# Performance work log

Hardware: AMD Instinct MI355X
Metric: run time of the kernel (lower is better)

Reference implementation:

```python
import jax, jax.numpy as jnp
import numpy as np

C = 512
C8 = C // 8   # query/key dim = 64
C2 = C // 2   # value dim = 256


def setup_inputs() -> dict:
    key = jax.random.key(0)
    ks = jax.random.split(key, 10)
    B, H, W = 4, 64, 64
    x = jax.random.normal(ks[0], (B, H, W, C), dtype=jnp.float32)
    # 1x1 conv kernels expressed as [in_ch, out_ch] matrices + biases
    Wf = jax.random.normal(ks[1], (C, C8), dtype=jnp.float32) * 0.02
    bf = jnp.zeros((C8,), dtype=jnp.float32)
    Wg = jax.random.normal(ks[2], (C, C8), dtype=jnp.float32) * 0.02
    bg = jnp.zeros((C8,), dtype=jnp.float32)
    Wh = jax.random.normal(ks[3], (C, C2), dtype=jnp.float32) * 0.02
    bh = jnp.zeros((C2,), dtype=jnp.float32)
    Wo = jax.random.normal(ks[4], (C2, C), dtype=jnp.float32) * 0.02
    bo = jnp.zeros((C,), dtype=jnp.float32)
    gamma = jax.random.normal(ks[5], (1,), dtype=jnp.float32) * 0.05
    return {"x": x, "Wf": Wf, "bf": bf, "Wg": Wg, "bg": bg,
            "Wh": Wh, "bh": bh, "Wo": Wo, "bo": bo, "gamma": gamma}


def reference(x, Wf, bf, Wg, bg, Wh, bh, Wo, bo, gamma):
    B, H, W, _ = x.shape
    N = H * W
    xf = x.reshape(B, N, C)                               # flatten spatial dims
    f = xf @ Wf + bf                                      # [B, N, C8] keys
    g = xf @ Wg + bg                                      # [B, N, C8] queries
    h = xf @ Wh + bh                                      # [B, N, C2] values
    s = jnp.einsum('bnd,bmd->bnm', g, f)                  # [B, N, N] scores (g @ f^T)
    beta = jax.nn.softmax(s, axis=-1)                     # attention map
    o = jnp.einsum('bnm,bmd->bnd', beta, h)               # [B, N, C2]
    o = o @ Wo + bo                                       # [B, N, C] output 1x1 conv
    out = gamma * o + xf                                  # residual with learned scale
    return out.reshape(B, H, W, C)
```

## Files before the change

kernel.cpp:

```cpp
#include <hip/hip_runtime.h>
#include <math.h>

#define B_   4
#define N_   4096
#define C_   512
#define C8_  64
#define C2_  256

typedef __attribute__((ext_vector_type(8))) short bf16x8;
typedef __attribute__((ext_vector_type(4))) short bf16x4;
typedef __attribute__((ext_vector_type(4))) float floatx4;
typedef __attribute__((ext_vector_type(16))) float floatx16;

__device__ __forceinline__ short f2bf(float x) {
    unsigned u = __float_as_uint(x);
    u += 0x7fff + ((u >> 16) & 1);
    return (short)(u >> 16);
}
__device__ __forceinline__ unsigned pack2bf(float a, float b) {
    return (unsigned)(unsigned short)f2bf(a) | ((unsigned)(unsigned short)f2bf(b) << 16);
}

union U8 { bf16x8 v; unsigned u[4]; };

__global__ __launch_bounds__(256) void convert_w(
    const float* __restrict__ Wf, const float* __restrict__ Wg,
    const float* __restrict__ Wh, const float* __restrict__ Wo,
    short* __restrict__ WcatT, short* __restrict__ WoT)
{
    int tid = blockIdx.x * 256 + threadIdx.x;
    if (tid < 384 * 512) {
        int n = tid >> 9, k = tid & 511;
        float v = (n < 64)  ? Wf[k * 64 + n]
                : (n < 128) ? Wg[k * 64 + (n - 64)]
                            : Wh[k * 256 + (n - 128)];
        WcatT[tid] = f2bf(v);
    } else {
        int t2 = tid - 384 * 512;
        int n = t2 >> 8, k = t2 & 255;
        WoT[t2] = f2bf(Wo[k * 512 + n]);
    }
}

__global__ __launch_bounds__(256, 2) void qkv_mfma(
    const float* __restrict__ x, const short* __restrict__ WcatT,
    const float* __restrict__ bfv, const float* __restrict__ bgv,
    const float* __restrict__ bhv,
    short* __restrict__ fbf, short* __restrict__ gbf, short* __restrict__ hT)
{
    const int ny = blockIdx.x;
    const int m0 = blockIdx.y * 128;
    const int n0 = ny * 128;
    const int t  = threadIdx.x;
    const int w  = t >> 6, lane = t & 63;
    const int l15 = lane & 15, quad = lane >> 4;
    const int wm = w & 1, wn = w >> 1;

    __shared__ short As[128 * 40];
    __shared__ short Bs[128 * 40];

    floatx4 acc[4][4];
    #pragma unroll
    for (int i = 0; i < 4; i++)
        #pragma unroll
        for (int j = 0; j < 4; j++) acc[i][j] = (floatx4){0.f,0.f,0.f,0.f};

    for (int k0 = 0; k0 < C_; k0 += 32) {
        #pragma unroll
        for (int i = 0; i < 4; i++) {
            int c = t + i * 256;
            int row = c >> 3, ko = (c & 7) * 4;
            float4 v = *(const float4*)&x[(size_t)(m0 + row) * C_ + k0 + ko];
            bf16x4 pk = { f2bf(v.x), f2bf(v.y), f2bf(v.z), f2bf(v.w) };
            *(bf16x4*)&As[row * 40 + ko] = pk;
        }
        #pragma unroll
        for (int i = 0; i < 2; i++) {
            int c = t + i * 256;
            int nr = c >> 2, ko = (c & 3) * 8;
            *(bf16x8*)&Bs[nr * 40 + ko] =
                *(const bf16x8*)&WcatT[(size_t)(n0 + nr) * 512 + k0 + ko];
        }
        __syncthreads();

        bf16x8 af[4], bfr[4];
        #pragma unroll
        for (int mt = 0; mt < 4; mt++)
            af[mt] = *(const bf16x8*)&As[(wm * 64 + mt * 16 + l15) * 40 + quad * 8];
        #pragma unroll
        for (int nt = 0; nt < 4; nt++)
            bfr[nt] = *(const bf16x8*)&Bs[(wn * 64 + nt * 16 + l15) * 40 + quad * 8];
        #pragma unroll
        for (int mt = 0; mt < 4; mt++)
            #pragma unroll
            for (int nt = 0; nt < 4; nt++)
                acc[mt][nt] = __builtin_amdgcn_mfma_f32_16x16x32_bf16(af[mt], bfr[nt], acc[mt][nt], 0, 0, 0);
        __syncthreads();
    }

    if (ny == 0) {
        #pragma unroll
        for (int mt = 0; mt < 4; mt++) {
            #pragma unroll
            for (int nt = 0; nt < 4; nt++) {
                int cn = wn * 64 + nt * 16 + l15;
                #pragma unroll
                for (int rg = 0; rg < 4; rg++) {
                    int row = m0 + wm * 64 + mt * 16 + quad * 4 + rg;
                    float v = acc[mt][nt][rg];
                    if (cn < 64) fbf[(size_t)row * 64 + cn]        = f2bf(v + bfv[cn]);
                    else         gbf[(size_t)row * 64 + (cn - 64)] = f2bf(v + bgv[cn - 64]);
                }
            }
        }
    } else {
        #pragma unroll
        for (int mt = 0; mt < 4; mt++) {
            #pragma unroll
            for (int nt = 0; nt < 4; nt++) {
                int hch = (ny - 1) * 128 + wn * 64 + nt * 16 + l15;
                int row = m0 + wm * 64 + mt * 16 + quad * 4;
                int bb = row >> 12, n = row & 4095;
                float bias = bhv[hch];
                bf16x4 pk = { f2bf(acc[mt][nt][0] + bias), f2bf(acc[mt][nt][1] + bias),
                              f2bf(acc[mt][nt][2] + bias), f2bf(acc[mt][nt][3] + bias) };
                *(bf16x4*)&hT[((size_t)(bb * 256 + hch)) * 4096 + n] = pk;
            }
        }
    }
}

#define HST 40

__global__ __launch_bounds__(256, 1) void attn_v3(
    const short* __restrict__ fK,
    const short* __restrict__ gQ,
    const short* __restrict__ hT,
    float* __restrict__ oPart,
    float* __restrict__ lPart)
{
    const int bx = blockIdx.x;
    const int s  = bx & 1;
    const int qt = (bx >> 1) & 31;
    const int b  = bx >> 6;
    const int kb = s * 2048;
    const int t  = threadIdx.x;
    const int w  = t >> 6, lane = t & 63;
    const int l31 = lane & 31, h = lane >> 5;
    const int wq = w & 1, wv = w >> 1;
    const int q_wave = qt * 128 + wq * 64;

    __shared__ short fs[2][64 * HST];
    __shared__ short hs[2][256 * HST];

    bf16x8 qf[2][4];
    #pragma unroll
    for (int n2 = 0; n2 < 2; n2++)
        #pragma unroll
        for (int k = 0; k < 4; k++)
            qf[n2][k] = *(const bf16x8*)&gQ[(size_t)(b * N_ + q_wave + n2 * 32 + l31) * 64 + k * 16 + h * 8];

    floatx16 oacc[2][4];
    #pragma unroll
    for (int n2 = 0; n2 < 2; n2++)
        #pragma unroll
        for (int vt = 0; vt < 4; vt++)
            #pragma unroll
            for (int j = 0; j < 16; j++) oacc[n2][vt][j] = 0.f;
    float lsum[2] = {0.f, 0.f};

    const int f_row = t >> 2, f_c = (t & 3) * 16;
    const int h_row = t >> 3, h_c = (t & 7) * 8;

    {
        *(bf16x8*)&fs[0][f_row * HST + f_c] =
            *(const bf16x8*)&fK[(size_t)(b * N_ + kb + f_row) * 64 + f_c];
        *(bf16x8*)&fs[0][f_row * HST + f_c + 8] =
            *(const bf16x8*)&fK[(size_t)(b * N_ + kb + f_row) * 64 + f_c + 8];
        #pragma unroll
        for (int i = 0; i < 8; i++)
            *(bf16x8*)&hs[0][(h_row + i * 32) * HST + h_c] =
                *(const bf16x8*)&hT[((size_t)(b * 256 + h_row + i * 32)) * 4096 + kb + h_c];
    }
    __syncthreads();

    for (int it = 0; it < 32; ++it) {
        const int cur = it & 1;
        const bool more = (it < 31);
        const int kn = kb + (it + 1) * 64;

        bf16x8 rf0, rf1, rh[8];
        if (more) {
            rf0 = *(const bf16x8*)&fK[(size_t)(b * N_ + kn + f_row) * 64 + f_c];
            rf1 = *(const bf16x8*)&fK[(size_t)(b * N_ + kn + f_row) * 64 + f_c + 8];
            #pragma unroll
            for (int i = 0; i < 8; i++)
                rh[i] = *(const bf16x8*)&hT[((size_t)(b * 256 + h_row + i * 32)) * 4096 + kn + h_c];
        }

        bf16x8 ffr[2][4];
        #pragma unroll
        for (int m = 0; m < 2; m++)
            #pragma unroll
            for (int k = 0; k < 4; k++)
                ffr[m][k] = *(const bf16x8*)&fs[cur][(m * 32 + l31) * HST + k * 16 + h * 8];

        floatx16 sacc[2][2];
        #pragma unroll
        for (int m = 0; m < 2; m++)
            #pragma unroll
            for (int n2 = 0; n2 < 2; n2++) {
                #pragma unroll
                for (int j = 0; j < 16; j++) sacc[m][n2][j] = 0.f;
                #pragma unroll
                for (int k = 0; k < 4; k++)
                    sacc[m][n2] = __builtin_amdgcn_mfma_f32_32x32x16_bf16(
                        ffr[m][k], qf[n2][k], sacc[m][n2], 0, 0, 0);
            }

        bf16x8 pfrag[2][4];
        #pragma unroll
        for (int m = 0; m < 2; m++)
            #pragma unroll
            for (int n2 = 0; n2 < 2; n2++) {
                float p[16]; float ps_ = 0.f;
                #pragma unroll
                for (int j = 0; j < 16; j++) { p[j] = __expf(sacc[m][n2][j]); ps_ += p[j]; }
                ps_ += __shfl_xor(ps_, 32);
                lsum[n2] += ps_;
                unsigned pk[8], xk[8];
                #pragma unroll
                for (int i = 0; i < 8; i++) pk[i] = pack2bf(p[2 * i], p[2 * i + 1]);
                #pragma unroll
                for (int i = 0; i < 8; i++) xk[i] = __shfl_xor(pk[i], 32);
                #pragma unroll
                for (int kp = 0; kp < 2; kp++) {
                    U8 u;
                    u.u[0] = h ? xk[4 * kp + 2] : pk[4 * kp];
                    u.u[1] = h ? xk[4 * kp + 3] : pk[4 * kp + 1];
                    u.u[2] = h ? pk[4 * kp + 2] : xk[4 * kp];
                    u.u[3] = h ? pk[4 * kp + 3] : xk[4 * kp + 1];
                    pfrag[n2][m * 2 + kp] = u.v;
                }
            }

        #pragma unroll
        for (int kk = 0; kk < 4; kk++)
            #pragma unroll
            for (int vt = 0; vt < 4; vt++) {
                bf16x8 vfr = *(const bf16x8*)&hs[cur][(wv * 128 + vt * 32 + l31) * HST + kk * 16 + h * 8];
                #pragma unroll
                for (int n2 = 0; n2 < 2; n2++)
                    oacc[n2][vt] = __builtin_amdgcn_mfma_f32_32x32x16_bf16(
                        pfrag[n2][kk], vfr, oacc[n2][vt], 0, 0, 0);
            }

        if (more) {
            const int nxt = cur ^ 1;
            *(bf16x8*)&fs[nxt][f_row * HST + f_c] = rf0;
            *(bf16x8*)&fs[nxt][f_row * HST + f_c + 8] = rf1;
            #pragma unroll
            for (int i = 0; i < 8; i++)
                *(bf16x8*)&hs[nxt][(h_row + i * 32) * HST + h_c] = rh[i];
        }
        __syncthreads();
    }

    #pragma unroll
    for (int n2 = 0; n2 < 2; n2++) {
        #pragma unroll
        for (int vt = 0; vt < 4; vt++) {
            int vch = wv * 128 + vt * 32 + l31;
            #pragma unroll
            for (int r = 0; r < 16; r++) {
                int q = q_wave + n2 * 32 + (r & 3) + 8 * (r >> 2) + 4 * h;
                oPart[(size_t)s * 4194304 + (size_t)(b * N_ + q) * 256 + vch] = oacc[n2][vt][r];
            }
        }
    }
    if (wv == 0 && lane < 32) {
        #pragma unroll
        for (int n2 = 0; n2 < 2; n2++)
            lPart[(size_t)s * 16384 + b * N_ + q_wave + n2 * 32 + lane] = lsum[n2];
    }
}

__global__ __launch_bounds__(256) void attn_combine(
    const float* __restrict__ oPart, const float* __restrict__ lPart,
    short* __restrict__ obf)
{
    int idx = blockIdx.x * 256 + threadIdx.x;
    int row = idx >> 6;
    int c4  = (idx & 63) << 2;
    float4 a = *(const float4*)&oPart[(size_t)row * 256 + c4];
    float4 b = *(const float4*)&oPart[4194304 + (size_t)row * 256 + c4];
    float inv = 1.0f / (lPart[row] + lPart[16384 + row]);
    bf16x4 o = { f2bf((a.x + b.x) * inv), f2bf((a.y + b.y) * inv),
                 f2bf((a.z + b.z) * inv), f2bf((a.w + b.w) * inv) };
    *(bf16x4*)&obf[(size_t)row * 256 + c4] = o;
}

__global__ __launch_bounds__(256, 2) void out_mfma(
    const short* __restrict__ obf, const short* __restrict__ WoT,
    const float* __restrict__ bo, const float* __restrict__ x,
    const float* __restrict__ gamma, float* __restrict__ out)
{
    const int n0 = blockIdx.x * 128;
    const int m0 = blockIdx.y * 128;
    const int t  = threadIdx.x;
    const int w  = t >> 6, lane = t & 63;
    const int l15 = lane & 15, quad = lane >> 4;
    const int wm = w & 1, wn = w >> 1;

    __shared__ short As[128 * 40];
    __shared__ short Bs[128 * 40];

    floatx4 acc[4][4];
    #pragma unroll
    for (int i = 0; i < 4; i++)
        #pragma unroll
        for (int j = 0; j < 4; j++) acc[i][j] = (floatx4){0.f,0.f,0.f,0.f};

    for (int k0 = 0; k0 < C2_; k0 += 32) {
        #pragma unroll
        for (int i = 0; i < 2; i++) {
            int c = t + i * 256;
            int row = c >> 2, ko = (c & 3) * 8;
            *(bf16x8*)&As[row * 40 + ko] =
                *(const bf16x8*)&obf[(size_t)(m0 + row) * 256 + k0 + ko];
        }
        #pragma unroll
        for (int i = 0; i < 2; i++) {
            int c = t + i * 256;
            int nr = c >> 2, ko = (c & 3) * 8;
            *(bf16x8*)&Bs[nr * 40 + ko] =
                *(const bf16x8*)&WoT[(size_t)(n0 + nr) * 256 + k0 + ko];
        }
        __syncthreads();

        bf16x8 af[4], bfr[4];
        #pragma unroll
        for (int mt = 0; mt < 4; mt++)
            af[mt] = *(const bf16x8*)&As[(wm * 64 + mt * 16 + l15) * 40 + quad * 8];
        #pragma unroll
        for (int nt = 0; nt < 4; nt++)
            bfr[nt] = *(const bf16x8*)&Bs[(wn * 64 + nt * 16 + l15) * 40 + quad * 8];
        #pragma unroll
        for (int mt = 0; mt < 4; mt++)
            #pragma unroll
            for (int nt = 0; nt < 4; nt++)
                acc[mt][nt] = __builtin_amdgcn_mfma_f32_16x16x32_bf16(af[mt], bfr[nt], acc[mt][nt], 0, 0, 0);
        __syncthreads();
    }

    const float gm = gamma[0];
    #pragma unroll
    for (int mt = 0; mt < 4; mt++) {
        #pragma unroll
        for (int nt = 0; nt < 4; nt++) {
            int col = n0 + wn * 64 + nt * 16 + l15;
            float bias = bo[col];
            #pragma unroll
            for (int rg = 0; rg < 4; rg++) {
                int row = m0 + wm * 64 + mt * 16 + quad * 4 + rg;
                out[(size_t)row * C_ + col] =
                    gm * (acc[mt][nt][rg] + bias) + x[(size_t)row * C_ + col];
            }
        }
    }
}

extern "C" void kernel_launch(void* const* d_in, const int* in_sizes, int n_in,
                              void* d_out, int out_size, void* d_ws, size_t ws_size,
                              hipStream_t stream) {
    (void)in_sizes; (void)n_in; (void)out_size; (void)ws_size;

    const float* x     = (const float*)d_in[0];
    const float* Wf    = (const float*)d_in[1];
    const float* bfv   = (const float*)d_in[2];
    const float* Wg    = (const float*)d_in[3];
    const float* bgv   = (const float*)d_in[4];
    const float* Wh    = (const float*)d_in[5];
    const float* bhv   = (const float*)d_in[6];
    const float* Wo    = (const float*)d_in[7];
    const float* bo    = (const float*)d_in[8];
    const float* gamma = (const float*)d_in[9];
    float* out = (float*)d_out;

    short* fbf   = (short*)d_ws;
    short* gbf   = fbf   + (size_t)B_ * N_ * C8_;
    short* hT    = gbf   + (size_t)B_ * N_ * C8_;
    short* obf   = hT    + (size_t)B_ * C2_ * N_;
    short* WcatT = obf   + (size_t)B_ * N_ * C2_;
    short* WoT   = WcatT + (size_t)384 * 512;
    float* oPart = (float*)(WoT + (size_t)512 * 256);
    float* lPart = oPart + (size_t)2 * 16384 * 256;

    convert_w<<<1280, 256, 0, stream>>>(Wf, Wg, Wh, Wo, WcatT, WoT);
    qkv_mfma<<<dim3(3, 128), 256, 0, stream>>>(x, WcatT, bfv, bgv, bhv, fbf, gbf, hT);
    attn_v3<<<256, 256, 0, stream>>>(fbf, gbf, hT, oPart, lPart);
    attn_combine<<<4096, 256, 0, stream>>>(oPart, lPart, obf);
    out_mfma<<<dim3(4, 128), 256, 0, stream>>>(obf, WoT, bo, x, gamma, out);
}
```

Measured before the change: 231.9 us.

## Split attention keys four ways, store bf16 partials, use exp2 with prescaled queries

The attention kernel now splits the key range into four chunks instead of two, giving 512 blocks, and allows two blocks per CU. Partial outputs are stored as bf16 instead of fp32, and the combine kernel sums four partials. Queries are prescaled by log2(e) so exp2f can replace __expf. P is packed to bf16 with a cheaper round-half-up permute, and the S/PV loop is interleaved per key half to lower register pressure and overlap the LDS stores. The aim is better occupancy and less partial-output traffic, at the cost of extra combine reads and some bf16 rounding in the partials. The softmax still has no max subtraction, as before.

Result: slower. 260.8 us (+12.5%).

```diff
diff --git a/kernel.cpp b/kernel.cpp
--- a/kernel.cpp
+++ b/kernel.cpp
@@ -6,6 +6,7 @@
 #define C_   512
 #define C8_  64
 #define C2_  256
+#define LOG2E 1.44269504f
 
 typedef __attribute__((ext_vector_type(8))) short bf16x8;
 typedef __attribute__((ext_vector_type(4))) short bf16x4;
@@ -17,8 +18,13 @@
     u += 0x7fff + ((u >> 16) & 1);
     return (short)(u >> 16);
 }
-__device__ __forceinline__ unsigned pack2bf(float a, float b) {
-    return (unsigned)(unsigned short)f2bf(a) | ((unsigned)(unsigned short)f2bf(b) << 16);
+__device__ __forceinline__ unsigned pack2bf_fast(float a, float b) {
+    unsigned ua = __float_as_uint(a) + 0x8000u;
+    unsigned ub = __float_as_uint(b) + 0x8000u;
+    return __builtin_amdgcn_perm(ub, ua, 0x07060302u);
+}
+__device__ __forceinline__ float bf2f(short s) {
+    return __uint_as_float(((unsigned)(unsigned short)s) << 16);
 }
 
 union U8 { bf16x8 v; unsigned u[4]; };
@@ -109,7 +115,7 @@
                     int row = m0 + wm * 64 + mt * 16 + quad * 4 + rg;
                     float v = acc[mt][nt][rg];
                     if (cn < 64) fbf[(size_t)row * 64 + cn]        = f2bf(v + bfv[cn]);
-                    else         gbf[(size_t)row * 64 + (cn - 64)] = f2bf(v + bgv[cn - 64]);
+                    else         gbf[(size_t)row * 64 + (cn - 64)] = f2bf((v + bgv[cn - 64]) * LOG2E);
                 }
             }
         }
@@ -132,18 +138,18 @@
 
 #define HST 40
 
-__global__ __launch_bounds__(256, 1) void attn_v3(
+__global__ __launch_bounds__(256, 2) void attn_v4(
     const short* __restrict__ fK,
     const short* __restrict__ gQ,
     const short* __restrict__ hT,
-    float* __restrict__ oPart,
+    short* __restrict__ oPartB,
     float* __restrict__ lPart)
 {
     const int bx = blockIdx.x;
-    const int s  = bx & 1;
-    const int qt = (bx >> 1) & 31;
-    const int b  = bx >> 6;
-    const int kb = s * 2048;
+    const int s  = bx & 3;
+    const int qt = (bx >> 2) & 31;
+    const int b  = bx >> 7;
+    const int kb = s * 1024;
     const int t  = threadIdx.x;
     const int w  = t >> 6, lane = t & 63;
     const int l31 = lane & 31, h = lane >> 5;
@@ -184,9 +190,9 @@
     }
     __syncthreads();
 
-    for (int it = 0; it < 32; ++it) {
+    for (int it = 0; it < 16; ++it) {
         const int cur = it & 1;
-        const bool more = (it < 31);
+        const bool more = (it < 15);
         const int kn = kb + (it + 1) * 64;
 
         bf16x8 rf0, rf1, rh[8];
@@ -198,39 +204,36 @@
                 rh[i] = *(const bf16x8*)&hT[((size_t)(b * 256 + h_row + i * 32)) * 4096 + kn + h_c];
         }
 
-        bf16x8 ffr[2][4];
-        #pragma unroll
-        for (int m = 0; m < 2; m++)
+        #pragma unroll
+        for (int m = 0; m < 2; m++) {
+            bf16x8 ffr[4];
             #pragma unroll
             for (int k = 0; k < 4; k++)
-                ffr[m][k] = *(const bf16x8*)&fs[cur][(m * 32 + l31) * HST + k * 16 + h * 8];
-
-        floatx16 sacc[2][2];
-        #pragma unroll
-        for (int m = 0; m < 2; m++)
-            #pragma unroll
-            for (int n2 = 0; n2 < 2; n2++) {
-                #pragma unroll
-                for (int j = 0; j < 16; j++) sacc[m][n2][j] = 0.f;
-                #pragma unroll
-                for (int k = 0; k < 4; k++)
-                    sacc[m][n2] = __builtin_amdgcn_mfma_f32_32x32x16_bf16(
-                        ffr[m][k], qf[n2][k], sacc[m][n2], 0, 0, 0);
-            }
-
-        bf16x8 pfrag[2][4];
-        #pragma unroll
-        for (int m = 0; m < 2; m++)
+                ffr[k] = *(const bf16x8*)&fs[cur][(m * 32 + l31) * HST + k * 16 + h * 8];
+
+            floatx16 sacc[2];
+            #pragma unroll
+            for (int n2 = 0; n2 < 2; n2++)
+                #pragma unroll
+                for (int j = 0; j < 16; j++) sacc[n2][j] = 0.f;
+            #pragma unroll
+            for (int k = 0; k < 4; k++)
+                #pragma unroll
+                for (int n2 = 0; n2 < 2; n2++)
+                    sacc[n2] = __builtin_amdgcn_mfma_f32_32x32x16_bf16(
+                        ffr[k], qf[n2][k], sacc[n2], 0, 0, 0);
+
+            bf16x8 pf[2][2];
             #pragma unroll
             for (int n2 = 0; n2 < 2; n2++) {
                 float p[16]; float ps_ = 0.f;
                 #pragma unroll
-                for (int j = 0; j < 16; j++) { p[j] = __expf(sacc[m][n2][j]); ps_ += p[j]; }
+                for (int j = 0; j < 16; j++) { p[j] = exp2f(sacc[n2][j]); ps_ += p[j]; }
                 ps_ += __shfl_xor(ps_, 32);
                 lsum[n2] += ps_;
                 unsigned pk[8], xk[8];
                 #pragma unroll
-                for (int i = 0; i < 8; i++) pk[i] = pack2bf(p[2 * i], p[2 * i + 1]);
+                for (int i = 0; i < 8; i++) pk[i] = pack2bf_fast(p[2 * i], p[2 * i + 1]);
                 #pragma unroll
                 for (int i = 0; i < 8; i++) xk[i] = __shfl_xor(pk[i], 32);
                 #pragma unroll
@@ -240,28 +243,31 @@
                     u.u[1] = h ? xk[4 * kp + 3] : pk[4 * kp + 1];
                     u.u[2] = h ? pk[4 * kp + 2] : xk[4 * kp];
                     u.u[3] = h ? pk[4 * kp + 3] : xk[4 * kp + 1];
-                    pfrag[n2][m * 2 + kp] = u.v;
+                    pf[n2][kp] = u.v;
                 }
             }
 
-        #pragma unroll
-        for (int kk = 0; kk < 4; kk++)
-            #pragma unroll
-            for (int vt = 0; vt < 4; vt++) {
-                bf16x8 vfr = *(const bf16x8*)&hs[cur][(wv * 128 + vt * 32 + l31) * HST + kk * 16 + h * 8];
-                #pragma unroll
-                for (int n2 = 0; n2 < 2; n2++)
-                    oacc[n2][vt] = __builtin_amdgcn_mfma_f32_32x32x16_bf16(
-                        pfrag[n2][kk], vfr, oacc[n2][vt], 0, 0, 0);
-            }
-
-        if (more) {
-            const int nxt = cur ^ 1;
-            *(bf16x8*)&fs[nxt][f_row * HST + f_c] = rf0;
-            *(bf16x8*)&fs[nxt][f_row * HST + f_c + 8] = rf1;
-            #pragma unroll
-            for (int i = 0; i < 8; i++)
-                *(bf16x8*)&hs[nxt][(h_row + i * 32) * HST + h_c] = rh[i];
+            if (m == 1 && more) {
+                const int nxt = cur ^ 1;
+                *(bf16x8*)&fs[nxt][f_row * HST + f_c] = rf0;
+                *(bf16x8*)&fs[nxt][f_row * HST + f_c + 8] = rf1;
+                #pragma unroll
+                for (int i = 0; i < 8; i++)
+                    *(bf16x8*)&hs[nxt][(h_row + i * 32) * HST + h_c] = rh[i];
+            }
+
+            #pragma unroll
+            for (int kp = 0; kp < 2; kp++) {
+                const int kk = m * 2 + kp;
+                #pragma unroll
+                for (int vt = 0; vt < 4; vt++) {
+                    bf16x8 vfr = *(const bf16x8*)&hs[cur][(wv * 128 + vt * 32 + l31) * HST + kk * 16 + h * 8];
+                    #pragma unroll
+                    for (int n2 = 0; n2 < 2; n2++)
+                        oacc[n2][vt] = __builtin_amdgcn_mfma_f32_32x32x16_bf16(
+                            pf[n2][kp], vfr, oacc[n2][vt], 0, 0, 0);
+                }
+            }
         }
         __syncthreads();
     }
@@ -274,7 +280,7 @@
             #pragma unroll
             for (int r = 0; r < 16; r++) {
                 int q = q_wave + n2 * 32 + (r & 3) + 8 * (r >> 2) + 4 * h;
-                oPart[(size_t)s * 4194304 + (size_t)(b * N_ + q) * 256 + vch] = oacc[n2][vt][r];
+                oPartB[(size_t)s * 4194304 + (size_t)(b * N_ + q) * 256 + vch] = f2bf(oacc[n2][vt][r]);
             }
         }
     }
@@ -286,18 +292,25 @@
 }
 
 __global__ __launch_bounds__(256) void attn_combine(
-    const float* __restrict__ oPart, const float* __restrict__ lPart,
+    const short* __restrict__ oPartB, const float* __restrict__ lPart,
     short* __restrict__ obf)
 {
     int idx = blockIdx.x * 256 + threadIdx.x;
-    int row = idx >> 6;
-    int c4  = (idx & 63) << 2;
-    float4 a = *(const float4*)&oPart[(size_t)row * 256 + c4];
-    float4 b = *(const float4*)&oPart[4194304 + (size_t)row * 256 + c4];
-    float inv = 1.0f / (lPart[row] + lPart[16384 + row]);
-    bf16x4 o = { f2bf((a.x + b.x) * inv), f2bf((a.y + b.y) * inv),
-                 f2bf((a.z + b.z) * inv), f2bf((a.w + b.w) * inv) };
-    *(bf16x4*)&obf[(size_t)row * 256 + c4] = o;
+    int row = idx >> 5;
+    int c8  = (idx & 31) << 3;
+    float acc[8] = {0.f,0.f,0.f,0.f,0.f,0.f,0.f,0.f};
+    #pragma unroll
+    for (int s = 0; s < 4; s++) {
+        bf16x8 v = *(const bf16x8*)&oPartB[(size_t)s * 4194304 + (size_t)row * 256 + c8];
+        #pragma unroll
+        for (int j = 0; j < 8; j++) acc[j] += bf2f(v[j]);
+    }
+    float inv = 1.0f / (lPart[row] + lPart[16384 + row] +
+                        lPart[32768 + row] + lPart[49152 + row]);
+    bf16x8 o;
+    #pragma unroll
+    for (int j = 0; j < 8; j++) o[j] = f2bf(acc[j] * inv);
+    *(bf16x8*)&obf[(size_t)row * 256 + c8] = o;
 }
 
 __global__ __launch_bounds__(256, 2) void out_mfma(
@@ -387,18 +400,18 @@
     const float* gamma = (const float*)d_in[9];
     float* out = (float*)d_out;
 
-    short* fbf   = (short*)d_ws;
-    short* gbf   = fbf   + (size_t)B_ * N_ * C8_;
-    short* hT    = gbf   + (size_t)B_ * N_ * C8_;
-    short* obf   = hT    + (size_t)B_ * C2_ * N_;
-    short* WcatT = obf   + (size_t)B_ * N_ * C2_;
-    short* WoT   = WcatT + (size_t)384 * 512;
-    float* oPart = (float*)(WoT + (size_t)512 * 256);
-    float* lPart = oPart + (size_t)2 * 16384 * 256;
+    short* fbf    = (short*)d_ws;
+    short* gbf    = fbf    + (size_t)B_ * N_ * C8_;
+    short* hT     = gbf    + (size_t)B_ * N_ * C8_;
+    short* obf    = hT     + (size_t)B_ * C2_ * N_;
+    short* WcatT  = obf    + (size_t)B_ * N_ * C2_;
+    short* WoT    = WcatT  + (size_t)384 * 512;
+    short* oPartB = WoT    + (size_t)512 * 256;
+    float* lPart  = (float*)(oPartB + (size_t)4 * 16384 * 256);
 
     convert_w<<<1280, 256, 0, stream>>>(Wf, Wg, Wh, Wo, WcatT, WoT);
     qkv_mfma<<<dim3(3, 128), 256, 0, stream>>>(x, WcatT, bfv, bgv, bhv, fbf, gbf, hT);
-    attn_v3<<<256, 256, 0, stream>>>(fbf, gbf, hT, oPart, lPart);
-    attn_combine<<<4096, 256, 0, stream>>>(oPart, lPart, obf);
+    attn_v4<<<512, 256, 0, stream>>>(fbf, gbf, hT, oPartB, lPart);
+    attn_combine<<<2048, 256, 0, stream>>>(oPartB, lPart, obf);
     out_mfma<<<dim3(4, 128), 256, 0, stream>>>(obf, WoT, bo, x, gamma, out);
 }
```
